# Kernel tuning notes

Measured on AMD Instinct MI355X. Metric: run time of the kernel, lower is better.

## Reference

```python
import jax, jax.numpy as jnp
import numpy as np

N_NODES = 20000
N_EDGES = 320000
D_IN = 256
D_HID = 256
D_OUT = 128
N_LAYERS = 5
BN_EPS = 1e-5
W_SCALE = 1.0 / np.sqrt(D_HID)


def setup_inputs() -> dict:
    key = jax.random.key(0)
    ks = jax.random.split(key, 16)
    x = jax.random.normal(ks[0], (N_NODES, D_IN), dtype=jnp.float32)
    edge_index = jax.random.randint(ks[1], (2, N_EDGES), 0, N_NODES, dtype=jnp.int32)
    W1 = jax.random.normal(ks[2], (N_LAYERS, D_IN, D_HID), dtype=jnp.float32) * W_SCALE
    b1 = jax.random.normal(ks[3], (N_LAYERS, D_HID), dtype=jnp.float32) * 0.01
    W2a = jax.random.normal(ks[4], (N_LAYERS - 1, D_HID, D_HID), dtype=jnp.float32) * W_SCALE
    b2a = jax.random.normal(ks[5], (N_LAYERS - 1, D_HID), dtype=jnp.float32) * 0.01
    W2_last = jax.random.normal(ks[6], (D_HID, D_OUT), dtype=jnp.float32) * W_SCALE
    b2_last = jax.random.normal(ks[7], (D_OUT,), dtype=jnp.float32) * 0.01
    eps = jnp.zeros((N_LAYERS,), dtype=jnp.float32)
    bn_gamma = jnp.ones((N_LAYERS - 1, D_HID), dtype=jnp.float32)
    bn_beta = jnp.zeros((N_LAYERS - 1, D_HID), dtype=jnp.float32)
    bn_mean = jax.random.normal(ks[8], (N_LAYERS - 1, D_HID), dtype=jnp.float32) * 0.1
    bn_var = jax.random.uniform(ks[9], (N_LAYERS - 1, D_HID), dtype=jnp.float32, minval=0.5, maxval=1.5)
    return {"x": x, "edge_index": edge_index, "W1": W1, "b1": b1, "W2a": W2a,
            "b2a": b2a, "W2_last": W2_last, "b2_last": b2_last, "eps": eps,
            "bn_gamma": bn_gamma, "bn_beta": bn_beta, "bn_mean": bn_mean, "bn_var": bn_var}


def reference(x, edge_index, W1, b1, W2a, b2a, W2_last, b2_last, eps,
              bn_gamma, bn_beta, bn_mean, bn_var):
    src, dst = edge_index[0], edge_index[1]
    n = x.shape[0]

    def gin_conv(h, e, w1, bb1, w2, bb2):
        # scatter-add neighbor sum: agg[v] = sum_{(u->v)} h[u]
        agg = jax.ops.segment_sum(h[src], dst, num_segments=n)  # [N, d]
        z = (1.0 + e) * h + agg
        z = jax.nn.relu(z @ w1 + bb1)
        return z @ w2 + bb2

    h = x
    for i in range(N_LAYERS - 1):
        h = gin_conv(h, eps[i], W1[i], b1[i], W2a[i], b2a[i])
        # BatchNorm1d in eval mode (running stats); dropout inactive at inference
        h = (h - bn_mean[i]) * jax.lax.rsqrt(bn_var[i] + BN_EPS) * bn_gamma[i] + bn_beta[i]
        h = jax.nn.relu(h)
    out = gin_conv(h, eps[N_LAYERS - 1], W1[N_LAYERS - 1], b1[N_LAYERS - 1], W2_last, b2_last)
    return out
```

## Files before the change

kernel.cpp:

```cpp
#include <hip/hip_runtime.h>
#include <stdint.h>

#define NN    20000
#define NE    320000
#define MPAD  20096
#define DD    256
#define DOUT  128
#define CAP   64
#define RS    40
#define SS    2568
#define STS   264
#define SFS   132

typedef unsigned short u16;
typedef __attribute__((ext_vector_type(8))) __bf16 bf16x8;
typedef __attribute__((ext_vector_type(4))) float  f32x4;

__device__ __forceinline__ u16 f2b(float f){
  union { float f; uint32_t u; } x; x.f = f;
  uint32_t r = x.u + 0x7FFFu + ((x.u >> 16) & 1u);
  return (u16)(r >> 16);
}
__device__ __forceinline__ float blo(uint32_t p){ union{uint32_t u;float f;}x; x.u=p<<16;         return x.f; }
__device__ __forceinline__ float bhi(uint32_t p){ union{uint32_t u;float f;}x; x.u=p&0xFFFF0000u; return x.f; }

#define TB 152
#define XB (MPAD/4)
#define EB ((NE+255)/256)
__global__ __launch_bounds__(256) void prep_all(
    const float* __restrict__ x, const int* __restrict__ src, const int* __restrict__ dst,
    const float* __restrict__ W1, const float* __restrict__ W2a, const float* __restrict__ W2l,
    u16* __restrict__ W1t, u16* __restrict__ W2at, u16* __restrict__ W2lt,
    u16* __restrict__ h0, int* __restrict__ cnt, int* __restrict__ csr)
{
  __shared__ u16 Ts[64][65];
  int b = blockIdx.x, tid = threadIdx.x;
  if (b < TB){
    const float* srcp; u16* dstp; int ldS, k0, n0;
    if (b < 80){
      int layer = b >> 4, sub = b & 15;
      srcp = W1 + layer*65536; dstp = W1t + layer*65536; ldS = 256;
      k0 = (sub >> 2)*64; n0 = (sub & 3)*64;
    } else if (b < 144){
      int bb = b - 80; int layer = bb >> 4, sub = bb & 15;
      srcp = W2a + layer*65536; dstp = W2at + layer*65536; ldS = 256;
      k0 = (sub >> 2)*64; n0 = (sub & 3)*64;
    } else {
      int sub = b - 144;
      srcp = W2l; dstp = W2lt; ldS = 128;
      k0 = (sub >> 1)*64; n0 = (sub & 1)*64;
    }
    int c = tid & 63, r0 = tid >> 6;
    #pragma unroll
    for (int i = 0; i < 16; ++i){
      int r = r0 + i*4;
      Ts[r][c] = f2b(srcp[(size_t)(k0 + r)*ldS + n0 + c]);
    }
    __syncthreads();
    #pragma unroll
    for (int i = 0; i < 16; ++i){
      int n = r0 + i*4;
      dstp[(size_t)(n0 + n)*256 + k0 + c] = Ts[c][n];
    }
  } else if (b < TB + XB){
    int bb = b - TB;
    int row  = bb*4 + (tid >> 6);
    int lane = tid & 63;
    uint2 o = make_uint2(0u, 0u);
    if (row < NN){
      float4 f = *(const float4*)(x + (size_t)row*DD + lane*4);
      o.x = (uint32_t)f2b(f.x) | ((uint32_t)f2b(f.y) << 16);
      o.y = (uint32_t)f2b(f.z) | ((uint32_t)f2b(f.w) << 16);
    }
    *(uint2*)(h0 + (size_t)row*DD + lane*4) = o;
  } else {
    int e = (b - TB - XB)*256 + tid;
    if (e < NE){
      int d = dst[e];
      int slot = atomicAdd(&cnt[d], 1);
      if (slot < CAP) csr[d*CAP + slot] = src[e];
    }
  }
}

__global__ __launch_bounds__(256) void gather(
    const u16* __restrict__ hin, const int* __restrict__ cnt, const int* __restrict__ csr,
    const float* __restrict__ eps_arr, int layer, u16* __restrict__ z)
{
  int w = threadIdx.x >> 6, lane = threadIdx.x & 63;
  int v = __builtin_amdgcn_readfirstlane(blockIdx.x*4 + w);
  float a0 = 0.f, a1 = 0.f, a2 = 0.f, a3 = 0.f;
  if (v < NN){
    float e = 1.0f + eps_arr[layer];
    uint2 ov = *(const uint2*)(hin + (size_t)v*DD + lane*4);
    int deg = cnt[v]; deg = deg > CAP ? CAP : deg;
    const int4* lq = (const int4*)(csr + (size_t)v*CAP);
    for (int base = 0; base < deg; base += 8){
      int4 q0 = lq[(base >> 2) + 0];
      int4 q1 = lq[(base >> 2) + 1];
      int nb[8] = { q0.x, q0.y, q0.z, q0.w, q1.x, q1.y, q1.z, q1.w };
      uint2 rv[8];
      #pragma unroll
      for (int c = 0; c < 8; ++c){
        int id = (base + c < deg) ? nb[c] : v;
        rv[c] = *(const uint2*)(hin + (size_t)id*DD + lane*4);
      }
      #pragma unroll
      for (int c = 0; c < 8; ++c){
        if (base + c < deg){
          a0 += blo(rv[c].x); a1 += bhi(rv[c].x);
          a2 += blo(rv[c].y); a3 += bhi(rv[c].y);
        }
      }
    }
    a0 += e*blo(ov.x); a1 += e*bhi(ov.x);
    a2 += e*blo(ov.y); a3 += e*bhi(ov.y);
  }
  uint2 o;
  o.x = (uint32_t)f2b(a0) | ((uint32_t)f2b(a1) << 16);
  o.y = (uint32_t)f2b(a2) | ((uint32_t)f2b(a3) << 16);
  *(uint2*)(z + (size_t)v*DD + lane*4) = o;
}

__global__ __launch_bounds__(256, 3) void mlp(
    const u16* __restrict__ z,
    const u16* __restrict__ w1, const float* __restrict__ b1,
    const u16* __restrict__ w2, const float* __restrict__ b2,
    const float* __restrict__ gma, const float* __restrict__ bta,
    const float* __restrict__ mu,  const float* __restrict__ var,
    u16* __restrict__ hout, float* __restrict__ outf, int last)
{
  __shared__ __align__(16) u16 As[8*SS];
  int tid  = threadIdx.x;
  int lane = tid & 63, w = tid >> 6;
  int m0 = blockIdx.x * 64;
  int l15 = lane & 15, l4 = lane >> 4;

  f32x4 acc1[4][4];
  #pragma unroll
  for (int i=0;i<4;++i)
    #pragma unroll
    for (int j=0;j<4;++j){ f32x4 zr={0.f,0.f,0.f,0.f}; acc1[i][j]=zr; }
  {
    int hidb = w*64;
    const u16* zb = z + (size_t)m0*DD;
    for (int s = 0; s < 8; ++s){
      bf16x8 af[4], bz[4];
      #pragma unroll
      for (int mi=0;mi<4;++mi)
        af[mi] = *(const bf16x8*)(w1 + (size_t)(hidb + mi*16 + l15)*DD + s*32 + l4*8);
      #pragma unroll
      for (int nj=0;nj<4;++nj)
        bz[nj] = *(const bf16x8*)(zb + (size_t)(nj*16 + l15)*DD + s*32 + l4*8);
      #pragma unroll
      for (int mi=0;mi<4;++mi)
        #pragma unroll
        for (int nj=0;nj<4;++nj)
          acc1[mi][nj] = __builtin_amdgcn_mfma_f32_16x16x32_bf16(af[mi], bz[nj], acc1[mi][nj], 0,0,0);
    }
  }

  {
    int hidb = w*64;
    #pragma unroll
    for (int mi=0;mi<4;++mi){
      float4 bv = *(const float4*)(b1 + hidb + mi*16 + l4*4);
      int s2 = w*2 + (mi >> 1);
      int kp = (mi & 1)*16 + l4*4;
      #pragma unroll
      for (int nj=0;nj<4;++nj){
        int zrow = nj*16 + l15;
        float v0 = acc1[mi][nj][0] + bv.x; v0 = v0 > 0.f ? v0 : 0.f;
        float v1 = acc1[mi][nj][1] + bv.y; v1 = v1 > 0.f ? v1 : 0.f;
        float v2 = acc1[mi][nj][2] + bv.z; v2 = v2 > 0.f ? v2 : 0.f;
        float v3 = acc1[mi][nj][3] + bv.w; v3 = v3 > 0.f ? v3 : 0.f;
        uint2 pk;
        pk.x = (uint32_t)f2b(v0) | ((uint32_t)f2b(v1) << 16);
        pk.y = (uint32_t)f2b(v2) | ((uint32_t)f2b(v3) << 16);
        *(uint2*)(As + s2*SS + zrow*RS + kp) = pk;
      }
    }
  }
  __syncthreads();

  if (!last){
    f32x4 acc2[4][4];
    #pragma unroll
    for (int i=0;i<4;++i)
      #pragma unroll
      for (int j=0;j<4;++j){ f32x4 zr={0.f,0.f,0.f,0.f}; acc2[i][j]=zr; }
    int cb = w*64;
    for (int s = 0; s < 8; ++s){
      bf16x8 at[4], bw[4];
      #pragma unroll
      for (int i=0;i<4;++i)
        at[i] = *(const bf16x8*)(As + s*SS + (i*16 + l15)*RS + l4*8);
      #pragma unroll
      for (int j=0;j<4;++j)
        bw[j] = *(const bf16x8*)(w2 + (size_t)(cb + j*16 + l15)*DD + s*32 + l4*8);
      #pragma unroll
      for (int i=0;i<4;++i)
        #pragma unroll
        for (int j=0;j<4;++j)
          acc2[i][j] = __builtin_amdgcn_mfma_f32_16x16x32_bf16(at[i], bw[j], acc2[i][j], 0,0,0);
    }
    __syncthreads();
    u16* St = As;
    #pragma unroll
    for (int j=0;j<4;++j){
      int col = cb + j*16 + l15;
      float sc = rsqrtf(var[col] + 1e-5f) * gma[col];
      float sh = (b2[col] - mu[col]) * sc + bta[col];
      #pragma unroll
      for (int i=0;i<4;++i){
        #pragma unroll
        for (int r=0;r<4;++r){
          int row = i*16 + l4*4 + r;
          float vv = acc2[i][j][r]*sc + sh;
          vv = vv > 0.f ? vv : 0.f;
          St[row*STS + col] = f2b(vv);
        }
      }
    }
    __syncthreads();
    #pragma unroll
    for (int it = 0; it < 8; ++it){
      int idx = it*256 + tid;
      int row = idx >> 5, c = idx & 31;
      *(uint4*)(hout + (size_t)(m0 + row)*DD + c*8) = *(const uint4*)(St + row*STS + c*8);
    }
  } else {
    f32x4 acc2[2][4];
    #pragma unroll
    for (int i=0;i<2;++i)
      #pragma unroll
      for (int j=0;j<4;++j){ f32x4 zr={0.f,0.f,0.f,0.f}; acc2[i][j]=zr; }
    int rh = (w >> 1)*32, cbk = (w & 1)*64;
    for (int s = 0; s < 8; ++s){
      bf16x8 at[2], bw[4];
      #pragma unroll
      for (int i=0;i<2;++i)
        at[i] = *(const bf16x8*)(As + s*SS + (rh + i*16 + l15)*RS + l4*8);
      #pragma unroll
      for (int j=0;j<4;++j)
        bw[j] = *(const bf16x8*)(w2 + (size_t)(cbk + j*16 + l15)*DD + s*32 + l4*8);
      #pragma unroll
      for (int i=0;i<2;++i)
        #pragma unroll
        for (int j=0;j<4;++j)
          acc2[i][j] = __builtin_amdgcn_mfma_f32_16x16x32_bf16(at[i], bw[j], acc2[i][j], 0,0,0);
    }
    __syncthreads();
    float* Sf = (float*)As;
    #pragma unroll
    for (int j=0;j<4;++j){
      int col = cbk + j*16 + l15;
      float sh = b2[col];
      #pragma unroll
      for (int i=0;i<2;++i){
        #pragma unroll
        for (int r=0;r<4;++r){
          int row = rh + i*16 + l4*4 + r;
          Sf[row*SFS + col] = acc2[i][j][r] + sh;
        }
      }
    }
    __syncthreads();
    #pragma unroll
    for (int it = 0; it < 8; ++it){
      int idx = it*256 + tid;
      int row = idx >> 5, c = idx & 31;
      if (m0 + row < NN)
        *(uint4*)(outf + (size_t)(m0 + row)*DOUT + c*4) = *(const uint4*)(Sf + row*SFS + c*4);
    }
  }
}

extern "C" void kernel_launch(void* const* d_in, const int* in_sizes, int n_in,
                              void* d_out, int out_size, void* d_ws, size_t ws_size,
                              hipStream_t stream)
{
  const float* x     = (const float*)d_in[0];
  const int*   ei    = (const int*)  d_in[1];
  const float* W1    = (const float*)d_in[2];
  const float* b1    = (const float*)d_in[3];
  const float* W2a   = (const float*)d_in[4];
  const float* b2a   = (const float*)d_in[5];
  const float* W2l   = (const float*)d_in[6];
  const float* b2l   = (const float*)d_in[7];
  const float* eps   = (const float*)d_in[8];
  const float* gma   = (const float*)d_in[9];
  const float* bta   = (const float*)d_in[10];
  const float* mu    = (const float*)d_in[11];
  const float* var   = (const float*)d_in[12];
  float* out = (float*)d_out;

  char* ws = (char*)d_ws;
  size_t off = 0;
  auto alloc = [&](size_t bytes)->void*{
    void* p = ws + off; off += (bytes + 255) & ~(size_t)255; return p;
  };
  u16* h0   = (u16*)alloc((size_t)MPAD*DD*2);
  u16* h1   = (u16*)alloc((size_t)MPAD*DD*2);
  u16* zb   = (u16*)alloc((size_t)MPAD*DD*2);
  int* cnt  = (int*)alloc((size_t)NN*4);
  int* csr  = (int*)alloc((size_t)NN*CAP*4 + 64);
  u16* W1t  = (u16*)alloc((size_t)5*65536*2);
  u16* W2at = (u16*)alloc((size_t)4*65536*2);
  u16* W2lt = (u16*)alloc((size_t)32768*2);

  const int* srcA = ei;
  const int* dstA = ei + NE;

  hipMemsetAsync(cnt, 0, (size_t)NN*4, stream);
  prep_all<<<TB + XB + EB, 256, 0, stream>>>(x, srcA, dstA, W1, W2a, W2l,
                                             W1t, W2at, W2lt, h0, cnt, csr);

  u16* hbuf[2] = { h0, h1 };
  for (int L = 0; L < 5; ++L){
    const u16* hin = hbuf[L & 1];
    u16*       ho  = hbuf[1 - (L & 1)];
    gather<<<MPAD/4, 256, 0, stream>>>(hin, cnt, csr, eps, L, zb);
    if (L < 4){
      mlp<<<MPAD/64, 256, 0, stream>>>(zb,
          W1t + (size_t)L*65536, b1 + L*256,
          W2at + (size_t)L*65536, b2a + L*256,
          gma + L*256, bta + L*256, mu + L*256, var + L*256,
          ho, nullptr, 0);
    } else {
      mlp<<<MPAD/64, 256, 0, stream>>>(zb,
          W1t + (size_t)L*65536, b1 + L*256,
          W2lt, b2l,
          nullptr, nullptr, nullptr, nullptr,
          nullptr, out, 1);
    }
  }
}
```

Baseline: 389.2 us.

## Fuse neighbor gather into MLP kernel and halve row tile to 32

Removes the separate gather kernel: each fused block aggregates neighbor features for its 32 rows directly into shared memory, then runs both GEMMs on them. This drops the write and re-read of the z intermediate buffer and one launch per layer. In exchange the row tile shrinks from 64 to 32, so W1/W2 weights are reloaded from global twice as often, and gather latency now sits inside the MFMA kernel with fewer waves available to hide it.

```diff
diff --git a/kernel.cpp b/kernel.cpp
--- a/kernel.cpp
+++ b/kernel.cpp
@@ -8,7 +8,7 @@
 #define DOUT  128
 #define CAP   64
 #define RS    40
-#define SS    2568
+#define SS    1288
 #define STS   264
 #define SFS   132
 
@@ -83,47 +83,9 @@
   }
 }
 
-__global__ __launch_bounds__(256) void gather(
+__global__ __launch_bounds__(256, 3) void gin_fused(
     const u16* __restrict__ hin, const int* __restrict__ cnt, const int* __restrict__ csr,
-    const float* __restrict__ eps_arr, int layer, u16* __restrict__ z)
-{
-  int w = threadIdx.x >> 6, lane = threadIdx.x & 63;
-  int v = __builtin_amdgcn_readfirstlane(blockIdx.x*4 + w);
-  float a0 = 0.f, a1 = 0.f, a2 = 0.f, a3 = 0.f;
-  if (v < NN){
-    float e = 1.0f + eps_arr[layer];
-    uint2 ov = *(const uint2*)(hin + (size_t)v*DD + lane*4);
-    int deg = cnt[v]; deg = deg > CAP ? CAP : deg;
-    const int4* lq = (const int4*)(csr + (size_t)v*CAP);
-    for (int base = 0; base < deg; base += 8){
-      int4 q0 = lq[(base >> 2) + 0];
-      int4 q1 = lq[(base >> 2) + 1];
-      int nb[8] = { q0.x, q0.y, q0.z, q0.w, q1.x, q1.y, q1.z, q1.w };
-      uint2 rv[8];
-      #pragma unroll
-      for (int c = 0; c < 8; ++c){
-        int id = (base + c < deg) ? nb[c] : v;
-        rv[c] = *(const uint2*)(hin + (size_t)id*DD + lane*4);
-      }
-      #pragma unroll
-      for (int c = 0; c < 8; ++c){
-        if (base + c < deg){
-          a0 += blo(rv[c].x); a1 += bhi(rv[c].x);
-          a2 += blo(rv[c].y); a3 += bhi(rv[c].y);
-        }
-      }
-    }
-    a0 += e*blo(ov.x); a1 += e*bhi(ov.x);
-    a2 += e*blo(ov.y); a3 += e*bhi(ov.y);
-  }
-  uint2 o;
-  o.x = (uint32_t)f2b(a0) | ((uint32_t)f2b(a1) << 16);
-  o.y = (uint32_t)f2b(a2) | ((uint32_t)f2b(a3) << 16);
-  *(uint2*)(z + (size_t)v*DD + lane*4) = o;
-}
-
-__global__ __launch_bounds__(256, 3) void mlp(
-    const u16* __restrict__ z,
+    const float* __restrict__ eps_arr, int layer,
     const u16* __restrict__ w1, const float* __restrict__ b1,
     const u16* __restrict__ w2, const float* __restrict__ b2,
     const float* __restrict__ gma, const float* __restrict__ bta,
@@ -133,32 +95,72 @@
   __shared__ __align__(16) u16 As[8*SS];
   int tid  = threadIdx.x;
   int lane = tid & 63, w = tid >> 6;
-  int m0 = blockIdx.x * 64;
+  int m0 = blockIdx.x * 32;
   int l15 = lane & 15, l4 = lane >> 4;
 
-  f32x4 acc1[4][4];
+  {
+    float e = 1.0f + eps_arr[layer];
+    u16* dstL = As + (lane >> 3)*SS + (lane & 7)*4;
+    for (int i = 0; i < 8; ++i){
+      int row = w*8 + i;
+      int v = __builtin_amdgcn_readfirstlane(m0 + row);
+      float a0 = 0.f, a1 = 0.f, a2 = 0.f, a3 = 0.f;
+      if (v < NN){
+        uint2 ov = *(const uint2*)(hin + (size_t)v*DD + lane*4);
+        int deg = cnt[v]; deg = deg > CAP ? CAP : deg;
+        const int4* lq = (const int4*)(csr + (size_t)v*CAP);
+        for (int base = 0; base < deg; base += 8){
+          int4 q0 = lq[(base >> 2) + 0];
+          int4 q1 = lq[(base >> 2) + 1];
+          int nb[8] = { q0.x, q0.y, q0.z, q0.w, q1.x, q1.y, q1.z, q1.w };
+          uint2 rv[8];
+          #pragma unroll
+          for (int c = 0; c < 8; ++c){
+            int id = (base + c < deg) ? nb[c] : v;
+            rv[c] = *(const uint2*)(hin + (size_t)id*DD + lane*4);
+          }
+          #pragma unroll
+          for (int c = 0; c < 8; ++c){
+            if (base + c < deg){
+              a0 += blo(rv[c].x); a1 += bhi(rv[c].x);
+              a2 += blo(rv[c].y); a3 += bhi(rv[c].y);
+            }
+          }
+        }
+        a0 += e*blo(ov.x); a1 += e*bhi(ov.x);
+        a2 += e*blo(ov.y); a3 += e*bhi(ov.y);
+      }
+      uint2 o;
+      o.x = (uint32_t)f2b(a0) | ((uint32_t)f2b(a1) << 16);
+      o.y = (uint32_t)f2b(a2) | ((uint32_t)f2b(a3) << 16);
+      *(uint2*)(dstL + row*RS) = o;
+    }
+  }
+  __syncthreads();
+
+  f32x4 acc1[4][2];
   #pragma unroll
   for (int i=0;i<4;++i)
     #pragma unroll
-    for (int j=0;j<4;++j){ f32x4 zr={0.f,0.f,0.f,0.f}; acc1[i][j]=zr; }
+    for (int j=0;j<2;++j){ f32x4 zr={0.f,0.f,0.f,0.f}; acc1[i][j]=zr; }
   {
     int hidb = w*64;
-    const u16* zb = z + (size_t)m0*DD;
     for (int s = 0; s < 8; ++s){
-      bf16x8 af[4], bz[4];
+      bf16x8 af[4], bz[2];
       #pragma unroll
       for (int mi=0;mi<4;++mi)
         af[mi] = *(const bf16x8*)(w1 + (size_t)(hidb + mi*16 + l15)*DD + s*32 + l4*8);
       #pragma unroll
-      for (int nj=0;nj<4;++nj)
-        bz[nj] = *(const bf16x8*)(zb + (size_t)(nj*16 + l15)*DD + s*32 + l4*8);
+      for (int nj=0;nj<2;++nj)
+        bz[nj] = *(const bf16x8*)(As + s*SS + (nj*16 + l15)*RS + l4*8);
       #pragma unroll
       for (int mi=0;mi<4;++mi)
         #pragma unroll
-        for (int nj=0;nj<4;++nj)
+        for (int nj=0;nj<2;++nj)
           acc1[mi][nj] = __builtin_amdgcn_mfma_f32_16x16x32_bf16(af[mi], bz[nj], acc1[mi][nj], 0,0,0);
     }
   }
+  __syncthreads();
 
   {
     int hidb = w*64;
@@ -168,7 +170,7 @@
       int s2 = w*2 + (mi >> 1);
       int kp = (mi & 1)*16 + l4*4;
       #pragma unroll
-      for (int nj=0;nj<4;++nj){
+      for (int nj=0;nj<2;++nj){
         int zrow = nj*16 + l15;
         float v0 = acc1[mi][nj][0] + bv.x; v0 = v0 > 0.f ? v0 : 0.f;
         float v1 = acc1[mi][nj][1] + bv.y; v1 = v1 > 0.f ? v1 : 0.f;
@@ -184,22 +186,22 @@
   __syncthreads();
 
   if (!last){
-    f32x4 acc2[4][4];
-    #pragma unroll
-    for (int i=0;i<4;++i)
+    f32x4 acc2[2][4];
+    #pragma unroll
+    for (int i=0;i<2;++i)
       #pragma unroll
       for (int j=0;j<4;++j){ f32x4 zr={0.f,0.f,0.f,0.f}; acc2[i][j]=zr; }
     int cb = w*64;
     for (int s = 0; s < 8; ++s){
-      bf16x8 at[4], bw[4];
-      #pragma unroll
-      for (int i=0;i<4;++i)
+      bf16x8 at[2], bw[4];
+      #pragma unroll
+      for (int i=0;i<2;++i)
         at[i] = *(const bf16x8*)(As + s*SS + (i*16 + l15)*RS + l4*8);
       #pragma unroll
       for (int j=0;j<4;++j)
         bw[j] = *(const bf16x8*)(w2 + (size_t)(cb + j*16 + l15)*DD + s*32 + l4*8);
       #pragma unroll
-      for (int i=0;i<4;++i)
+      for (int i=0;i<2;++i)
         #pragma unroll
         for (int j=0;j<4;++j)
           acc2[i][j] = __builtin_amdgcn_mfma_f32_16x16x32_bf16(at[i], bw[j], acc2[i][j], 0,0,0);
@@ -212,7 +214,7 @@
       float sc = rsqrtf(var[col] + 1e-5f) * gma[col];
       float sh = (b2[col] - mu[col]) * sc + bta[col];
       #pragma unroll
-      for (int i=0;i<4;++i){
+      for (int i=0;i<2;++i){
         #pragma unroll
         for (int r=0;r<4;++r){
           int row = i*16 + l4*4 + r;
@@ -224,50 +226,50 @@
     }
     __syncthreads();
     #pragma unroll
-    for (int it = 0; it < 8; ++it){
+    for (int it = 0; it < 4; ++it){
       int idx = it*256 + tid;
       int row = idx >> 5, c = idx & 31;
       *(uint4*)(hout + (size_t)(m0 + row)*DD + c*8) = *(const uint4*)(St + row*STS + c*8);
     }
   } else {
-    f32x4 acc2[2][4];
+    f32x4 acc2[2][2];
     #pragma unroll
     for (int i=0;i<2;++i)
       #pragma unroll
-      for (int j=0;j<4;++j){ f32x4 zr={0.f,0.f,0.f,0.f}; acc2[i][j]=zr; }
-    int rh = (w >> 1)*32, cbk = (w & 1)*64;
+      for (int j=0;j<2;++j){ f32x4 zr={0.f,0.f,0.f,0.f}; acc2[i][j]=zr; }
+    int cbk = w*32;
     for (int s = 0; s < 8; ++s){
-      bf16x8 at[2], bw[4];
+      bf16x8 at[2], bw[2];
       #pragma unroll
       for (int i=0;i<2;++i)
-        at[i] = *(const bf16x8*)(As + s*SS + (rh + i*16 + l15)*RS + l4*8);
-      #pragma unroll
-      for (int j=0;j<4;++j)
+        at[i] = *(const bf16x8*)(As + s*SS + (i*16 + l15)*RS + l4*8);
+      #pragma unroll
+      for (int j=0;j<2;++j)
         bw[j] = *(const bf16x8*)(w2 + (size_t)(cbk + j*16 + l15)*DD + s*32 + l4*8);
       #pragma unroll
       for (int i=0;i<2;++i)
         #pragma unroll
-        for (int j=0;j<4;++j)
+        for (int j=0;j<2;++j)
           acc2[i][j] = __builtin_amdgcn_mfma_f32_16x16x32_bf16(at[i], bw[j], acc2[i][j], 0,0,0);
     }
     __syncthreads();
     float* Sf = (float*)As;
     #pragma unroll
-    for (int j=0;j<4;++j){
+    for (int j=0;j<2;++j){
       int col = cbk + j*16 + l15;
       float sh = b2[col];
       #pragma unroll
       for (int i=0;i<2;++i){
         #pragma unroll
         for (int r=0;r<4;++r){
-          int row = rh + i*16 + l4*4 + r;
+          int row = i*16 + l4*4 + r;
           Sf[row*SFS + col] = acc2[i][j][r] + sh;
         }
       }
     }
     __syncthreads();
     #pragma unroll
-    for (int it = 0; it < 8; ++it){
+    for (int it = 0; it < 4; ++it){
       int idx = it*256 + tid;
       int row = idx >> 5, c = idx & 31;
       if (m0 + row < NN)
@@ -302,7 +304,6 @@
   };
   u16* h0   = (u16*)alloc((size_t)MPAD*DD*2);
   u16* h1   = (u16*)alloc((size_t)MPAD*DD*2);
-  u16* zb   = (u16*)alloc((size_t)MPAD*DD*2);
   int* cnt  = (int*)alloc((size_t)NN*4);
   int* csr  = (int*)alloc((size_t)NN*CAP*4 + 64);
   u16* W1t  = (u16*)alloc((size_t)5*65536*2);
@@ -320,15 +321,14 @@
   for (int L = 0; L < 5; ++L){
     const u16* hin = hbuf[L & 1];
     u16*       ho  = hbuf[1 - (L & 1)];
-    gather<<<MPAD/4, 256, 0, stream>>>(hin, cnt, csr, eps, L, zb);
     if (L < 4){
-      mlp<<<MPAD/64, 256, 0, stream>>>(zb,
+      gin_fused<<<MPAD/32, 256, 0, stream>>>(hin, cnt, csr, eps, L,
           W1t + (size_t)L*65536, b1 + L*256,
           W2at + (size_t)L*65536, b2a + L*256,
           gma + L*256, bta + L*256, mu + L*256, var + L*256,
           ho, nullptr, 0);
     } else {
-      mlp<<<MPAD/64, 256, 0, stream>>>(zb,
+      gin_fused<<<MPAD/32, 256, 0, stream>>>(hin, cnt, csr, eps, L,
           W1t + (size_t)L*65536, b1 + L*256,
           W2lt, b2l,
           nullptr, nullptr, nullptr, nullptr,
```

Result: faster. 349.2 us (-10.3%).

## Split gather into feature slices with half-wave neighbor parallelism

Applied to the files above, without the earlier changes.

The gather kernel is restructured so that each block handles one 64-column feature slice (4 slices) for 128 nodes. Each wave processes 32 nodes two at a time, and the two half-waves split the neighbor list and are combined with ds_bpermute. The aim is a smaller per-block working set for L2/cache locality and more memory-level parallelism per wave. The trade-off is 4-byte loads instead of 8-byte, redundant CSR reads across slices, and extra cross-lane reductions. The cnt/csr buffers are padded to MPAD to allow the vectorized degree loads.

```diff
diff --git a/kernel.cpp b/kernel.cpp
--- a/kernel.cpp
+++ b/kernel.cpp
@@ -7,6 +7,8 @@
 #define DD    256
 #define DOUT  128
 #define CAP   64
+#define NSL   4
+#define SLW   64
 #define RS    40
 #define SS    2568
 #define STS   264
@@ -16,13 +18,15 @@
 typedef __attribute__((ext_vector_type(8))) __bf16 bf16x8;
 typedef __attribute__((ext_vector_type(4))) float  f32x4;
 
-__device__ __forceinline__ u16 f2b(float f){
+__device__ __forceinline__ uint32_t f2b(float f){
   union { float f; uint32_t u; } x; x.f = f;
   uint32_t r = x.u + 0x7FFFu + ((x.u >> 16) & 1u);
-  return (u16)(r >> 16);
+  return r >> 16;
 }
 __device__ __forceinline__ float blo(uint32_t p){ union{uint32_t u;float f;}x; x.u=p<<16;         return x.f; }
 __device__ __forceinline__ float bhi(uint32_t p){ union{uint32_t u;float f;}x; x.u=p&0xFFFF0000u; return x.f; }
+__device__ __forceinline__ int   fiu(float f){ union{float f;int i;}x; x.f=f; return x.i; }
+__device__ __forceinline__ float uif(int i){ union{int i;float f;}x; x.i=i; return x.f; }
 
 #define TB 152
 #define XB (MPAD/4)
@@ -54,7 +58,7 @@
     #pragma unroll
     for (int i = 0; i < 16; ++i){
       int r = r0 + i*4;
-      Ts[r][c] = f2b(srcp[(size_t)(k0 + r)*ldS + n0 + c]);
+      Ts[r][c] = (u16)f2b(srcp[(size_t)(k0 + r)*ldS + n0 + c]);
     }
     __syncthreads();
     #pragma unroll
@@ -69,8 +73,8 @@
     uint2 o = make_uint2(0u, 0u);
     if (row < NN){
       float4 f = *(const float4*)(x + (size_t)row*DD + lane*4);
-      o.x = (uint32_t)f2b(f.x) | ((uint32_t)f2b(f.y) << 16);
-      o.y = (uint32_t)f2b(f.z) | ((uint32_t)f2b(f.w) << 16);
+      o.x = f2b(f.x) | (f2b(f.y) << 16);
+      o.y = f2b(f.z) | (f2b(f.w) << 16);
     }
     *(uint2*)(h0 + (size_t)row*DD + lane*4) = o;
   } else {
@@ -87,39 +91,102 @@
     const u16* __restrict__ hin, const int* __restrict__ cnt, const int* __restrict__ csr,
     const float* __restrict__ eps_arr, int layer, u16* __restrict__ z)
 {
-  int w = threadIdx.x >> 6, lane = threadIdx.x & 63;
-  int v = __builtin_amdgcn_readfirstlane(blockIdx.x*4 + w);
-  float a0 = 0.f, a1 = 0.f, a2 = 0.f, a3 = 0.f;
-  if (v < NN){
-    float e = 1.0f + eps_arr[layer];
-    uint2 ov = *(const uint2*)(hin + (size_t)v*DD + lane*4);
-    int deg = cnt[v]; deg = deg > CAP ? CAP : deg;
-    const int4* lq = (const int4*)(csr + (size_t)v*CAP);
-    for (int base = 0; base < deg; base += 8){
-      int4 q0 = lq[(base >> 2) + 0];
-      int4 q1 = lq[(base >> 2) + 1];
-      int nb[8] = { q0.x, q0.y, q0.z, q0.w, q1.x, q1.y, q1.z, q1.w };
-      uint2 rv[8];
+  int tid = threadIdx.x, lane = tid & 63, w = tid >> 6;
+  int s = blockIdx.x & 3, chunk = blockIdx.x >> 2;
+  int half = lane >> 5, kl = lane & 31;
+  int xi = (lane ^ 32) << 2;
+  float e = 1.0f + eps_arr[layer];
+  int v0 = chunk*128 + w*32;
+  const u16* hs = hin + s*SLW + kl*2;
+  u16*       zs = z   + s*SLW + kl*2;
+  int dg[32];
+  {
+    const int4* cq = (const int4*)(cnt + v0);
+    #pragma unroll
+    for (int c = 0; c < 8; ++c){
+      int4 cc = cq[c];
+      dg[4*c+0] = cc.x; dg[4*c+1] = cc.y; dg[4*c+2] = cc.z; dg[4*c+3] = cc.w;
+    }
+  }
+  #pragma unroll 1
+  for (int p = 0; p < 16; ++p){
+    int va = v0 + 2*p, vb = va + 1;
+    int da = dg[2*p];   da = da > CAP ? CAP : da;
+    int db = dg[2*p+1]; db = db > CAP ? CAP : db;
+    const int4* lqa = (const int4*)(csr + (size_t)va*CAP);
+    const int4* lqb = (const int4*)(csr + (size_t)vb*CAP);
+    int4 qa[4], qb[4];
+    #pragma unroll
+    for (int c = 0; c < 4; ++c){ qa[c] = lqa[c]; qb[c] = lqb[c]; }
+    float a0=0.f, a1=0.f, b0=0.f, b1=0.f;
+    uint32_t ra[8], rb[8];
+    int ia[8], ib[8];
+    #pragma unroll
+    for (int c = 0; c < 4; ++c){
+      ia[2*c]   = half ? qa[c].y : qa[c].x;  ia[2*c+1] = half ? qa[c].w : qa[c].z;
+      ib[2*c]   = half ? qb[c].y : qb[c].x;  ib[2*c+1] = half ? qb[c].w : qb[c].z;
+    }
+    #pragma unroll
+    for (int c = 0; c < 8; ++c){
+      int ga = (2*c + half < da) ? ia[c] : va;
+      int gb = (2*c + half < db) ? ib[c] : vb;
+      ra[c] = *(const uint32_t*)(hs + (size_t)ga*DD);
+      rb[c] = *(const uint32_t*)(hs + (size_t)gb*DD);
+    }
+    #pragma unroll
+    for (int c = 0; c < 8; ++c){
+      if (2*c + half < da){ a0 += blo(ra[c]); a1 += bhi(ra[c]); }
+      if (2*c + half < db){ b0 += blo(rb[c]); b1 += bhi(rb[c]); }
+    }
+    for (int base = 16; base < da; base += 16){
+      int4 q[4];
+      #pragma unroll
+      for (int c = 0; c < 4; ++c) q[c] = lqa[(base >> 2) + c];
+      int id[8];
+      #pragma unroll
+      for (int c = 0; c < 4; ++c){ id[2*c] = half ? q[c].y : q[c].x; id[2*c+1] = half ? q[c].w : q[c].z; }
+      uint32_t rv[8];
       #pragma unroll
       for (int c = 0; c < 8; ++c){
-        int id = (base + c < deg) ? nb[c] : v;
-        rv[c] = *(const uint2*)(hin + (size_t)id*DD + lane*4);
+        int g = (base + 2*c + half < da) ? id[c] : va;
+        rv[c] = *(const uint32_t*)(hs + (size_t)g*DD);
       }
       #pragma unroll
+      for (int c = 0; c < 8; ++c)
+        if (base + 2*c + half < da){ a0 += blo(rv[c]); a1 += bhi(rv[c]); }
+    }
+    for (int base = 16; base < db; base += 16){
+      int4 q[4];
+      #pragma unroll
+      for (int c = 0; c < 4; ++c) q[c] = lqb[(base >> 2) + c];
+      int id[8];
+      #pragma unroll
+      for (int c = 0; c < 4; ++c){ id[2*c] = half ? q[c].y : q[c].x; id[2*c+1] = half ? q[c].w : q[c].z; }
+      uint32_t rv[8];
+      #pragma unroll
       for (int c = 0; c < 8; ++c){
-        if (base + c < deg){
-          a0 += blo(rv[c].x); a1 += bhi(rv[c].x);
-          a2 += blo(rv[c].y); a3 += bhi(rv[c].y);
-        }
+        int g = (base + 2*c + half < db) ? id[c] : vb;
+        rv[c] = *(const uint32_t*)(hs + (size_t)g*DD);
       }
-    }
-    a0 += e*blo(ov.x); a1 += e*bhi(ov.x);
-    a2 += e*blo(ov.y); a3 += e*bhi(ov.y);
-  }
-  uint2 o;
-  o.x = (uint32_t)f2b(a0) | ((uint32_t)f2b(a1) << 16);
-  o.y = (uint32_t)f2b(a2) | ((uint32_t)f2b(a3) << 16);
-  *(uint2*)(z + (size_t)v*DD + lane*4) = o;
+      #pragma unroll
+      for (int c = 0; c < 8; ++c)
+        if (base + 2*c + half < db){ b0 += blo(rv[c]); b1 += bhi(rv[c]); }
+    }
+    uint32_t oa = *(const uint32_t*)(hs + (size_t)va*DD);
+    uint32_t ob = *(const uint32_t*)(hs + (size_t)vb*DD);
+    float ea = (half == 0 && va < NN) ? e : 0.0f;
+    float eb = (half == 0 && vb < NN) ? e : 0.0f;
+    a0 += ea*blo(oa); a1 += ea*bhi(oa);
+    b0 += eb*blo(ob); b1 += eb*bhi(ob);
+    a0 += uif(__builtin_amdgcn_ds_bpermute(xi, fiu(a0)));
+    a1 += uif(__builtin_amdgcn_ds_bpermute(xi, fiu(a1)));
+    b0 += uif(__builtin_amdgcn_ds_bpermute(xi, fiu(b0)));
+    b1 += uif(__builtin_amdgcn_ds_bpermute(xi, fiu(b1)));
+    if (half == 0){
+      *(uint32_t*)(zs + (size_t)va*DD) = f2b(a0) | (f2b(a1) << 16);
+      *(uint32_t*)(zs + (size_t)vb*DD) = f2b(b0) | (f2b(b1) << 16);
+    }
+  }
 }
 
 __global__ __launch_bounds__(256, 3) void mlp(
@@ -175,8 +242,8 @@
         float v2 = acc1[mi][nj][2] + bv.z; v2 = v2 > 0.f ? v2 : 0.f;
         float v3 = acc1[mi][nj][3] + bv.w; v3 = v3 > 0.f ? v3 : 0.f;
         uint2 pk;
-        pk.x = (uint32_t)f2b(v0) | ((uint32_t)f2b(v1) << 16);
-        pk.y = (uint32_t)f2b(v2) | ((uint32_t)f2b(v3) << 16);
+        pk.x = f2b(v0) | (f2b(v1) << 16);
+        pk.y = f2b(v2) | (f2b(v3) << 16);
         *(uint2*)(As + s2*SS + zrow*RS + kp) = pk;
       }
     }
@@ -218,7 +285,7 @@
           int row = i*16 + l4*4 + r;
           float vv = acc2[i][j][r]*sc + sh;
           vv = vv > 0.f ? vv : 0.f;
-          St[row*STS + col] = f2b(vv);
+          St[row*STS + col] = (u16)f2b(vv);
         }
       }
     }
@@ -303,8 +370,8 @@
   u16* h0   = (u16*)alloc((size_t)MPAD*DD*2);
   u16* h1   = (u16*)alloc((size_t)MPAD*DD*2);
   u16* zb   = (u16*)alloc((size_t)MPAD*DD*2);
-  int* cnt  = (int*)alloc((size_t)NN*4);
-  int* csr  = (int*)alloc((size_t)NN*CAP*4 + 64);
+  int* cnt  = (int*)alloc((size_t)MPAD*4);
+  int* csr  = (int*)alloc((size_t)MPAD*CAP*4 + 64);
   u16* W1t  = (u16*)alloc((size_t)5*65536*2);
   u16* W2at = (u16*)alloc((size_t)4*65536*2);
   u16* W2lt = (u16*)alloc((size_t)32768*2);
@@ -312,7 +379,7 @@
   const int* srcA = ei;
   const int* dstA = ei + NE;
 
-  hipMemsetAsync(cnt, 0, (size_t)NN*4, stream);
+  hipMemsetAsync(cnt, 0, (size_t)MPAD*4, stream);
   prep_all<<<TB + XB + EB, 256, 0, stream>>>(x, srcA, dstA, W1, W2a, W2l,
                                              W1t, W2at, W2lt, h0, cnt, csr);
 
@@ -320,7 +387,7 @@
   for (int L = 0; L < 5; ++L){
     const u16* hin = hbuf[L & 1];
     u16*       ho  = hbuf[1 - (L & 1)];
-    gather<<<MPAD/4, 256, 0, stream>>>(hin, cnt, csr, eps, L, zb);
+    gather<<<NSL*(MPAD/128), 256, 0, stream>>>(hin, cnt, csr, eps, L, zb);
     if (L < 4){
       mlp<<<MPAD/64, 256, 0, stream>>>(zb,
           W1t + (size_t)L*65536, b1 + L*256,
```

Result: slower. 514.2 us (+32.1%).
